# Kernel optimization log

Hardware: AMD Instinct MI355X
Metric: run time of the kernel (lower is better)

## Reference

```python
import jax, jax.numpy as jnp
import numpy as np


def setup_inputs() -> dict:
    key = jax.random.key(0)
    k = jax.random.split(key, 6)
    N, F, C = 8192, 64, 10
    scale = 1.0 / np.sqrt(F)  # keep activations bounded through relu chain
    return {
        "A_tilde": jax.random.uniform(k[0], (N, N), dtype=jnp.float32),
        "emb": jax.random.normal(k[1], (N, F), dtype=jnp.float32),
        "W1": jax.random.normal(k[2], (F, F), dtype=jnp.float32) * scale,
        "W2": jax.random.normal(k[3], (F, F), dtype=jnp.float32) * scale,
        "Wc": jax.random.normal(k[4], (F, C), dtype=jnp.float32) * scale,
        "bc": jnp.zeros((C,), dtype=jnp.float32),
    }


def reference(A_tilde, emb, W1, W2, Wc, bc):
    # D_tilde = rowsum(A)^(-1/2), with inf -> 0 (nan_to_num posinf=0)
    s = A_tilde.sum(axis=1)
    d = jnp.where(s > 0, jax.lax.rsqrt(jnp.where(s > 0, s, 1.0)), 0.0)  # [N]
    x = emb
    for W in (W1, W2):
        hw = x @ W                          # [N, F] = H W
        # DAD @ HW computed as d * (A @ (d * HW)) -- same math as
        # diag(d) @ A @ diag(d) @ HW, without materializing NxN products
        x = jax.nn.relu(d[:, None] * (A_tilde @ (d[:, None] * hw)))
        # dropout is identity in eval mode
    logits = x @ Wc + bc                    # [N, C]
    return logits
```

## Files before the change

### kernel.cpp

```cpp
#include <hip/hip_runtime.h>
#include <stdint.h>

#define N 8192
#define FD 64
#define NC 10

typedef __attribute__((ext_vector_type(8))) __bf16 bf16x8;
typedef __attribute__((ext_vector_type(4))) float f32x4;

__device__ __forceinline__ unsigned short f2bf(float f) {
    unsigned u = __builtin_bit_cast(unsigned, f);
    u += 0x7fffu + ((u >> 16) & 1u);
    return (unsigned short)(u >> 16);
}

__global__ __launch_bounds__(256) void rowsum_cast(const float* __restrict__ A,
                                                   unsigned short* __restrict__ Abf,
                                                   float* __restrict__ dvec) {
    const int row = blockIdx.x;
    const int t = threadIdx.x;
    const float4* Arow = (const float4*)(A + (size_t)row * N);
    ushort4* Brow = (ushort4*)(Abf + (size_t)row * N);
    float s = 0.f;
#pragma unroll
    for (int i = 0; i < 8; i++) {
        int c4 = t + 256 * i;
        float4 v = Arow[c4];
        s += (v.x + v.y) + (v.z + v.w);
        ushort4 o;
        o.x = f2bf(v.x); o.y = f2bf(v.y); o.z = f2bf(v.z); o.w = f2bf(v.w);
        Brow[c4] = o;
    }
#pragma unroll
    for (int off = 32; off > 0; off >>= 1) s += __shfl_down(s, off, 64);
    __shared__ float red[4];
    if ((t & 63) == 0) red[t >> 6] = s;
    __syncthreads();
    if (t == 0) {
        float tot = (red[0] + red[1]) + (red[2] + red[3]);
        dvec[row] = tot > 0.f ? rsqrtf(tot) : 0.f;
    }
}

__global__ __launch_bounds__(256) void xw_scale(const float* __restrict__ x,
                                                const float* __restrict__ W,
                                                const float* __restrict__ dvec,
                                                unsigned short* __restrict__ yT) {
    __shared__ float Ws[64][65];
    __shared__ float Xs[64][65];
    __shared__ float Ysh[64][65];
    const int t = threadIdx.x;
    const int r0 = blockIdx.x * 64;
#pragma unroll
    for (int i = 0; i < 16; i++) {
        int idx = t + 256 * i;
        Ws[idx >> 6][idx & 63] = W[idx];
        Xs[idx >> 6][idx & 63] = x[(size_t)r0 * 64 + idx];
    }
    __syncthreads();
    const int f = t & 63, w = t >> 6;
#pragma unroll
    for (int rr = 0; rr < 16; rr++) {
        int r = w * 16 + rr;
        float acc = 0.f;
#pragma unroll
        for (int j = 0; j < 64; j++) acc += Xs[r][j] * Ws[j][f];
        Ysh[r][f] = dvec[r0 + r] * acc;
    }
    __syncthreads();
    const int rl = t & 63, fq = t >> 6;
#pragma unroll
    for (int ff = 0; ff < 16; ff++) {
        int fi = fq * 16 + ff;
        yT[(size_t)fi * N + r0 + rl] = f2bf(Ysh[rl][fi]);
    }
}

__global__ __launch_bounds__(256) void spmm(const unsigned short* __restrict__ Abf,
                                            const unsigned short* __restrict__ yT,
                                            float* __restrict__ partial) {
    constexpr int BM = 64, BK = 128, SK = 4;
    constexpr int KS = N / SK;
    __shared__ unsigned short As[BM * BK];
    __shared__ unsigned short Ys[64 * BK];
    const int t = threadIdx.x;
    const int m0 = blockIdx.x * BM;
    const int kbase = blockIdx.y * KS;
    const int lane = t & 63, w = t >> 6;
    const int quad = lane >> 4, lr = lane & 15;

    f32x4 acc[4];
#pragma unroll
    for (int nt = 0; nt < 4; nt++) { acc[nt].x = 0.f; acc[nt].y = 0.f; acc[nt].z = 0.f; acc[nt].w = 0.f; }

    for (int k0 = kbase; k0 < kbase + KS; k0 += BK) {
#pragma unroll
        for (int p = 0; p < 4; p++) {
            int q = p * 256 + t;
            int row = q >> 4, c = q & 15;
            float4 va = *(const float4*)(Abf + (size_t)(m0 + row) * N + k0 + c * 8);
            *(float4*)(As + (row * 16 + (c ^ (row & 15))) * 8) = va;
            float4 vy = *(const float4*)(yT + (size_t)row * N + k0 + c * 8);
            *(float4*)(Ys + (row * 16 + (c ^ (row & 15))) * 8) = vy;
        }
        __syncthreads();
#pragma unroll
        for (int kk = 0; kk < BK; kk += 32) {
            int cc = (kk >> 3) + quad;
            bf16x8 af = *(const bf16x8*)(As + ((w * 16 + lr) * 16 + (cc ^ lr)) * 8);
#pragma unroll
            for (int nt = 0; nt < 4; nt++) {
                bf16x8 bv = *(const bf16x8*)(Ys + ((nt * 16 + lr) * 16 + (cc ^ lr)) * 8);
                acc[nt] = __builtin_amdgcn_mfma_f32_16x16x32_bf16(af, bv, acc[nt], 0, 0, 0);
            }
        }
        __syncthreads();
    }
#pragma unroll
    for (int nt = 0; nt < 4; nt++) {
#pragma unroll
        for (int r = 0; r < 4; r++) {
            int m = m0 + w * 16 + quad * 4 + r;
            int fcol = nt * 16 + lr;
            partial[((size_t)blockIdx.y * N + m) * FD + fcol] = acc[nt][r];
        }
    }
}

__global__ __launch_bounds__(256) void combine_relu(const float4* __restrict__ partial,
                                                    const float* __restrict__ dvec,
                                                    float4* __restrict__ xout) {
    const int gid = blockIdx.x * 256 + threadIdx.x;
    constexpr int S4 = N * FD / 4;
    float4 a = partial[gid];
    float4 b = partial[gid + S4];
    float4 c = partial[gid + 2 * S4];
    float4 e = partial[gid + 3 * S4];
    float dm = dvec[gid >> 4];
    float4 o;
    o.x = fmaxf(0.f, dm * ((a.x + b.x) + (c.x + e.x)));
    o.y = fmaxf(0.f, dm * ((a.y + b.y) + (c.y + e.y)));
    o.z = fmaxf(0.f, dm * ((a.z + b.z) + (c.z + e.z)));
    o.w = fmaxf(0.f, dm * ((a.w + b.w) + (c.w + e.w)));
    xout[gid] = o;
}

__global__ __launch_bounds__(256) void logits_k(const float* __restrict__ x2,
                                                const float* __restrict__ Wc,
                                                const float* __restrict__ bc,
                                                float* __restrict__ out) {
    const int id = blockIdx.x * 256 + threadIdx.x;
    const int m = id / NC, c = id - m * NC;
    const float* xr = x2 + (size_t)m * FD;
    float acc = bc[c];
#pragma unroll
    for (int j = 0; j < 64; j++) acc += xr[j] * Wc[j * NC + c];
    out[id] = acc;
}

extern "C" void kernel_launch(void* const* d_in, const int* in_sizes, int n_in,
                              void* d_out, int out_size, void* d_ws, size_t ws_size,
                              hipStream_t stream) {
    const float* A   = (const float*)d_in[0];
    const float* emb = (const float*)d_in[1];
    const float* W1  = (const float*)d_in[2];
    const float* W2  = (const float*)d_in[3];
    const float* Wc  = (const float*)d_in[4];
    const float* bc  = (const float*)d_in[5];
    char* ws = (char*)d_ws;

    unsigned short* Abf  = (unsigned short*)(ws);
    float* dvec          = (float*)(ws + 134217728);
    unsigned short* yT   = (unsigned short*)(ws + 134250496);
    float* xbuf          = (float*)(ws + 135299072);
    float* partial       = (float*)(ws + 137396224);
    float* out           = (float*)d_out;

    rowsum_cast<<<N, 256, 0, stream>>>(A, Abf, dvec);

    xw_scale<<<N / 64, 256, 0, stream>>>(emb, W1, dvec, yT);
    spmm<<<dim3(N / 64, 4), 256, 0, stream>>>(Abf, yT, partial);
    combine_relu<<<N * FD / 4 / 256, 256, 0, stream>>>((const float4*)partial, dvec, (float4*)xbuf);

    xw_scale<<<N / 64, 256, 0, stream>>>(xbuf, W2, dvec, yT);
    spmm<<<dim3(N / 64, 4), 256, 0, stream>>>(Abf, yT, partial);
    combine_relu<<<N * FD / 4 / 256, 256, 0, stream>>>((const float4*)partial, dvec, (float4*)xbuf);

    logits_k<<<N * NC / 256, 256, 0, stream>>>(xbuf, Wc, bc, out);
}
```

Measured before the change: 474.6 us.

## Fuse combine with XW and logits, retile spmm with direct global-to-LDS loads

Merges the split-K reduction and ReLU into the following XW projection and into the final logits kernel, which removes the intermediate x buffer and two launches. The spmm now uses 128-row tiles with two MFMA row-tiles per wave, split-K of 8, and global_load_lds direct copies into LDS. The XW inner loop is restructured into a register-blocked 16-output-per-thread form. Doubling split-K doubles the size of the partial buffer that must be written and then reduced.

```diff
diff --git a/kernel.cpp b/kernel.cpp
--- a/kernel.cpp
+++ b/kernel.cpp
@@ -4,6 +4,9 @@
 #define N 8192
 #define FD 64
 #define NC 10
+#define SK 8
+#define BM 128
+#define BK 128
 
 typedef __attribute__((ext_vector_type(8))) __bf16 bf16x8;
 typedef __attribute__((ext_vector_type(4))) float f32x4;
@@ -12,6 +15,12 @@
     unsigned u = __builtin_bit_cast(unsigned, f);
     u += 0x7fffu + ((u >> 16) & 1u);
     return (unsigned short)(u >> 16);
+}
+
+__device__ __forceinline__ void g2l16(const void* g, void* l) {
+    __builtin_amdgcn_global_load_lds(
+        (const __attribute__((address_space(1))) unsigned int*)g,
+        (__attribute__((address_space(3))) unsigned int*)l, 16, 0, 0);
 }
 
 __global__ __launch_bounds__(256) void rowsum_cast(const float* __restrict__ A,
@@ -42,120 +51,185 @@
     }
 }
 
-__global__ __launch_bounds__(256) void xw_scale(const float* __restrict__ x,
-                                                const float* __restrict__ W,
-                                                const float* __restrict__ dvec,
-                                                unsigned short* __restrict__ yT) {
-    __shared__ float Ws[64][65];
-    __shared__ float Xs[64][65];
-    __shared__ float Ysh[64][65];
+__device__ __forceinline__ void xw_inner(const float (*Xs)[69], const float* Ws,
+                                         const float* __restrict__ dvec,
+                                         unsigned short* __restrict__ yT,
+                                         int r0, int t) {
+    const int l = t & 63, w = t >> 6;
+    float acc[16];
+#pragma unroll
+    for (int i = 0; i < 16; i++) acc[i] = 0.f;
+#pragma unroll 8
+    for (int j = 0; j < 64; j++) {
+        float xv = Xs[l][j];
+        const float4* wr = (const float4*)(Ws + j * 64 + w * 16);
+        float4 w0 = wr[0], w1 = wr[1], w2 = wr[2], w3 = wr[3];
+        acc[0] += xv * w0.x; acc[1] += xv * w0.y; acc[2] += xv * w0.z; acc[3] += xv * w0.w;
+        acc[4] += xv * w1.x; acc[5] += xv * w1.y; acc[6] += xv * w1.z; acc[7] += xv * w1.w;
+        acc[8] += xv * w2.x; acc[9] += xv * w2.y; acc[10] += xv * w2.z; acc[11] += xv * w2.w;
+        acc[12] += xv * w3.x; acc[13] += xv * w3.y; acc[14] += xv * w3.z; acc[15] += xv * w3.w;
+    }
+    float dl = dvec[r0 + l];
+#pragma unroll
+    for (int ff = 0; ff < 16; ff++)
+        yT[(size_t)(w * 16 + ff) * N + r0 + l] = f2bf(dl * acc[ff]);
+}
+
+__global__ __launch_bounds__(256) void xw_from_global(const float* __restrict__ x,
+                                                      const float* __restrict__ W,
+                                                      const float* __restrict__ dvec,
+                                                      unsigned short* __restrict__ yT) {
+    __shared__ float Xs[64][69];
+    __shared__ __align__(16) float Ws[64 * 64];
     const int t = threadIdx.x;
     const int r0 = blockIdx.x * 64;
-#pragma unroll
-    for (int i = 0; i < 16; i++) {
-        int idx = t + 256 * i;
-        Ws[idx >> 6][idx & 63] = W[idx];
-        Xs[idx >> 6][idx & 63] = x[(size_t)r0 * 64 + idx];
-    }
-    __syncthreads();
-    const int f = t & 63, w = t >> 6;
-#pragma unroll
-    for (int rr = 0; rr < 16; rr++) {
-        int r = w * 16 + rr;
-        float acc = 0.f;
-#pragma unroll
-        for (int j = 0; j < 64; j++) acc += Xs[r][j] * Ws[j][f];
-        Ysh[r][f] = dvec[r0 + r] * acc;
-    }
-    __syncthreads();
-    const int rl = t & 63, fq = t >> 6;
-#pragma unroll
-    for (int ff = 0; ff < 16; ff++) {
-        int fi = fq * 16 + ff;
-        yT[(size_t)fi * N + r0 + rl] = f2bf(Ysh[rl][fi]);
-    }
+    const float4* x4 = (const float4*)x + (size_t)r0 * 16;
+    const float4* W4 = (const float4*)W;
+#pragma unroll
+    for (int p = 0; p < 4; p++) {
+        int idx = p * 256 + t;
+        ((float4*)Ws)[idx] = W4[idx];
+        float4 v = x4[idx];
+        int row = idx >> 4, f4 = (idx & 15) * 4;
+        Xs[row][f4] = v.x; Xs[row][f4 + 1] = v.y; Xs[row][f4 + 2] = v.z; Xs[row][f4 + 3] = v.w;
+    }
+    __syncthreads();
+    xw_inner(Xs, Ws, dvec, yT, r0, t);
 }
 
 __global__ __launch_bounds__(256) void spmm(const unsigned short* __restrict__ Abf,
                                             const unsigned short* __restrict__ yT,
                                             float* __restrict__ partial) {
-    constexpr int BM = 64, BK = 128, SK = 4;
     constexpr int KS = N / SK;
-    __shared__ unsigned short As[BM * BK];
-    __shared__ unsigned short Ys[64 * BK];
+    __shared__ __align__(16) unsigned short As[BM * BK];
+    __shared__ __align__(16) unsigned short Ys[64 * BK];
     const int t = threadIdx.x;
     const int m0 = blockIdx.x * BM;
     const int kbase = blockIdx.y * KS;
     const int lane = t & 63, w = t >> 6;
     const int quad = lane >> 4, lr = lane & 15;
 
-    f32x4 acc[4];
-#pragma unroll
-    for (int nt = 0; nt < 4; nt++) { acc[nt].x = 0.f; acc[nt].y = 0.f; acc[nt].z = 0.f; acc[nt].w = 0.f; }
+    f32x4 acc[2][4];
+#pragma unroll
+    for (int mt = 0; mt < 2; mt++)
+#pragma unroll
+        for (int nt = 0; nt < 4; nt++) {
+            acc[mt][nt].x = 0.f; acc[mt][nt].y = 0.f; acc[mt][nt].z = 0.f; acc[mt][nt].w = 0.f;
+        }
 
     for (int k0 = kbase; k0 < kbase + KS; k0 += BK) {
 #pragma unroll
+        for (int p = 0; p < 8; p++) {
+            int s = p * 256 + t;
+            int row = s >> 4, c = (s & 15) ^ (row & 15);
+            g2l16(Abf + (size_t)(m0 + row) * N + k0 + c * 8, As + s * 8);
+        }
+#pragma unroll
         for (int p = 0; p < 4; p++) {
-            int q = p * 256 + t;
-            int row = q >> 4, c = q & 15;
-            float4 va = *(const float4*)(Abf + (size_t)(m0 + row) * N + k0 + c * 8);
-            *(float4*)(As + (row * 16 + (c ^ (row & 15))) * 8) = va;
-            float4 vy = *(const float4*)(yT + (size_t)row * N + k0 + c * 8);
-            *(float4*)(Ys + (row * 16 + (c ^ (row & 15))) * 8) = vy;
+            int s = p * 256 + t;
+            int row = s >> 4, c = (s & 15) ^ (row & 15);
+            g2l16(yT + (size_t)row * N + k0 + c * 8, Ys + s * 8);
         }
         __syncthreads();
 #pragma unroll
         for (int kk = 0; kk < BK; kk += 32) {
             int cc = (kk >> 3) + quad;
-            bf16x8 af = *(const bf16x8*)(As + ((w * 16 + lr) * 16 + (cc ^ lr)) * 8);
+            bf16x8 af0 = *(const bf16x8*)(As + ((w * 32 + lr) * 16 + (cc ^ lr)) * 8);
+            bf16x8 af1 = *(const bf16x8*)(As + ((w * 32 + 16 + lr) * 16 + (cc ^ lr)) * 8);
 #pragma unroll
             for (int nt = 0; nt < 4; nt++) {
                 bf16x8 bv = *(const bf16x8*)(Ys + ((nt * 16 + lr) * 16 + (cc ^ lr)) * 8);
-                acc[nt] = __builtin_amdgcn_mfma_f32_16x16x32_bf16(af, bv, acc[nt], 0, 0, 0);
+                acc[0][nt] = __builtin_amdgcn_mfma_f32_16x16x32_bf16(af0, bv, acc[0][nt], 0, 0, 0);
+                acc[1][nt] = __builtin_amdgcn_mfma_f32_16x16x32_bf16(af1, bv, acc[1][nt], 0, 0, 0);
             }
         }
         __syncthreads();
     }
 #pragma unroll
-    for (int nt = 0; nt < 4; nt++) {
-#pragma unroll
-        for (int r = 0; r < 4; r++) {
-            int m = m0 + w * 16 + quad * 4 + r;
-            int fcol = nt * 16 + lr;
-            partial[((size_t)blockIdx.y * N + m) * FD + fcol] = acc[nt][r];
-        }
-    }
-}
-
-__global__ __launch_bounds__(256) void combine_relu(const float4* __restrict__ partial,
-                                                    const float* __restrict__ dvec,
-                                                    float4* __restrict__ xout) {
-    const int gid = blockIdx.x * 256 + threadIdx.x;
-    constexpr int S4 = N * FD / 4;
-    float4 a = partial[gid];
-    float4 b = partial[gid + S4];
-    float4 c = partial[gid + 2 * S4];
-    float4 e = partial[gid + 3 * S4];
-    float dm = dvec[gid >> 4];
-    float4 o;
-    o.x = fmaxf(0.f, dm * ((a.x + b.x) + (c.x + e.x)));
-    o.y = fmaxf(0.f, dm * ((a.y + b.y) + (c.y + e.y)));
-    o.z = fmaxf(0.f, dm * ((a.z + b.z) + (c.z + e.z)));
-    o.w = fmaxf(0.f, dm * ((a.w + b.w) + (c.w + e.w)));
-    xout[gid] = o;
-}
-
-__global__ __launch_bounds__(256) void logits_k(const float* __restrict__ x2,
-                                                const float* __restrict__ Wc,
-                                                const float* __restrict__ bc,
-                                                float* __restrict__ out) {
-    const int id = blockIdx.x * 256 + threadIdx.x;
-    const int m = id / NC, c = id - m * NC;
-    const float* xr = x2 + (size_t)m * FD;
-    float acc = bc[c];
-#pragma unroll
-    for (int j = 0; j < 64; j++) acc += xr[j] * Wc[j * NC + c];
-    out[id] = acc;
+    for (int mt = 0; mt < 2; mt++)
+#pragma unroll
+        for (int nt = 0; nt < 4; nt++)
+#pragma unroll
+            for (int r = 0; r < 4; r++) {
+                int m = m0 + w * 32 + mt * 16 + quad * 4 + r;
+                partial[((size_t)blockIdx.y * N + m) * FD + nt * 16 + lr] = acc[mt][nt][r];
+            }
+}
+
+__global__ __launch_bounds__(256) void combine_xw(const float4* __restrict__ partial4,
+                                                  const float* __restrict__ W,
+                                                  const float* __restrict__ dvec,
+                                                  unsigned short* __restrict__ yT) {
+    __shared__ float Xs[64][69];
+    __shared__ __align__(16) float Ws[64 * 64];
+    const int t = threadIdx.x;
+    const int r0 = blockIdx.x * 64;
+    const float4* W4 = (const float4*)W;
+#pragma unroll
+    for (int p = 0; p < 4; p++) {
+        int idx = p * 256 + t;
+        ((float4*)Ws)[idx] = W4[idx];
+        int row = idx >> 4, f4c = idx & 15;
+        size_t base = (size_t)(r0 + row) * 16 + f4c;
+        float4 s = partial4[base];
+#pragma unroll
+        for (int sk = 1; sk < SK; sk++) {
+            float4 v = partial4[(size_t)sk * (N * 16) + base];
+            s.x += v.x; s.y += v.y; s.z += v.z; s.w += v.w;
+        }
+        float dm = dvec[r0 + row];
+        int f4 = f4c * 4;
+        Xs[row][f4]     = fmaxf(0.f, dm * s.x);
+        Xs[row][f4 + 1] = fmaxf(0.f, dm * s.y);
+        Xs[row][f4 + 2] = fmaxf(0.f, dm * s.z);
+        Xs[row][f4 + 3] = fmaxf(0.f, dm * s.w);
+    }
+    __syncthreads();
+    xw_inner(Xs, Ws, dvec, yT, r0, t);
+}
+
+__global__ __launch_bounds__(256) void combine_logits(const float4* __restrict__ partial4,
+                                                      const float* __restrict__ dvec,
+                                                      const float* __restrict__ Wc,
+                                                      const float* __restrict__ bc,
+                                                      float* __restrict__ out) {
+    __shared__ float Xs[64][69];
+    __shared__ float Wcs[64][10];
+    __shared__ float bcs[10];
+    const int t = threadIdx.x;
+    const int r0 = blockIdx.x * 64;
+#pragma unroll
+    for (int p = 0; p < 4; p++) {
+        int idx = p * 256 + t;
+        int row = idx >> 4, f4c = idx & 15;
+        size_t base = (size_t)(r0 + row) * 16 + f4c;
+        float4 s = partial4[base];
+#pragma unroll
+        for (int sk = 1; sk < SK; sk++) {
+            float4 v = partial4[(size_t)sk * (N * 16) + base];
+            s.x += v.x; s.y += v.y; s.z += v.z; s.w += v.w;
+        }
+        float dm = dvec[r0 + row];
+        int f4 = f4c * 4;
+        Xs[row][f4]     = fmaxf(0.f, dm * s.x);
+        Xs[row][f4 + 1] = fmaxf(0.f, dm * s.y);
+        Xs[row][f4 + 2] = fmaxf(0.f, dm * s.z);
+        Xs[row][f4 + 3] = fmaxf(0.f, dm * s.w);
+    }
+    for (int i = t; i < 640; i += 256) Wcs[i / 10][i % 10] = Wc[i];
+    if (t < 10) bcs[t] = bc[t];
+    __syncthreads();
+#pragma unroll
+    for (int it = 0; it < 3; it++) {
+        int idx = it * 256 + t;
+        if (idx < 640) {
+            int r = idx / 10, c = idx - r * 10;
+            float acc = bcs[c];
+#pragma unroll
+            for (int j = 0; j < 64; j++) acc += Xs[r][j] * Wcs[j][c];
+            out[(size_t)(r0 + r) * NC + c] = acc;
+        }
+    }
 }
 
 extern "C" void kernel_launch(void* const* d_in, const int* in_sizes, int n_in,
@@ -172,19 +246,16 @@
     unsigned short* Abf  = (unsigned short*)(ws);
     float* dvec          = (float*)(ws + 134217728);
     unsigned short* yT   = (unsigned short*)(ws + 134250496);
-    float* xbuf          = (float*)(ws + 135299072);
-    float* partial       = (float*)(ws + 137396224);
+    float* partial       = (float*)(ws + 135299072);
     float* out           = (float*)d_out;
 
     rowsum_cast<<<N, 256, 0, stream>>>(A, Abf, dvec);
 
-    xw_scale<<<N / 64, 256, 0, stream>>>(emb, W1, dvec, yT);
-    spmm<<<dim3(N / 64, 4), 256, 0, stream>>>(Abf, yT, partial);
-    combine_relu<<<N * FD / 4 / 256, 256, 0, stream>>>((const float4*)partial, dvec, (float4*)xbuf);
-
-    xw_scale<<<N / 64, 256, 0, stream>>>(xbuf, W2, dvec, yT);
-    spmm<<<dim3(N / 64, 4), 256, 0, stream>>>(Abf, yT, partial);
-    combine_relu<<<N * FD / 4 / 256, 256, 0, stream>>>((const float4*)partial, dvec, (float4*)xbuf);
-
-    logits_k<<<N * NC / 256, 256, 0, stream>>>(xbuf, Wc, bc, out);
-}
+    xw_from_global<<<N / 64, 256, 0, stream>>>(emb, W1, dvec, yT);
+    spmm<<<dim3(N / BM, SK), 256, 0, stream>>>(Abf, yT, partial);
+
+    combine_xw<<<N / 64, 256, 0, stream>>>((const float4*)partial, W2, dvec, yT);
+    spmm<<<dim3(N / BM, SK), 256, 0, stream>>>(Abf, yT, partial);
+
+    combine_logits<<<N / 64, 256, 0, stream>>>((const float4*)partial, dvec, Wc, bc, out);
+}
```

New measurement: 451.5 us. 1.05x faster.
